# Performance work log

Hardware: AMD Instinct MI355X
Metric: run time of the kernel (lower is better)

## Reference

```python
import jax, jax.numpy as jnp
import numpy as np

N_NODES = 50000
N_EDGES = 800000
IN_F = 256
HEADS = 8
D = 32  # out_perhead
ALPHA_SLOPE = 0.2
EPS = 1e-16


def setup_inputs() -> dict:
    key = jax.random.key(0)
    k1, k2, k3, k4, k5 = jax.random.split(key, 5)
    x = jax.random.normal(k1, (N_NODES, IN_F), dtype=jnp.float32)
    W = jax.random.normal(k2, (HEADS, IN_F, D), dtype=jnp.float32) * 0.05
    a = jax.random.normal(k3, (HEADS, 5 * D), dtype=jnp.float32) * 0.05
    src = jax.random.randint(k4, (N_EDGES,), 0, N_NODES, dtype=jnp.int32)
    dst = jax.random.randint(k5, (N_EDGES,), 0, N_NODES, dtype=jnp.int32)
    return {"x": x, "W": W, "a": a, "src": src, "dst": dst}


def reference(x, W, a, src, dst):
    n = x.shape[0]
    # per-head projection: h[n, heads, d]
    h = jnp.einsum("ni,hio->nho", x, W)
    hs = h[src]  # [E, heads, d]  (edge[0] = source)
    hd = h[dst]  # [E, heads, d]  (edge[1] = destination)
    diff = hd - hs
    # a is the concat attention vector: [src | dst | diff | abs_diff | prod]
    a1, a2, a3, a4, a5 = jnp.split(a, 5, axis=1)  # each [heads, d]
    lin = (
        jnp.einsum("ehd,hd->eh", hs, a1)
        + jnp.einsum("ehd,hd->eh", hd, a2)
        + jnp.einsum("ehd,hd->eh", diff, a3)
        + jnp.einsum("ehd,hd->eh", jnp.abs(diff), a4)
        + jnp.einsum("ehd,hd->eh", hs * hd, a5)
    )  # [E, heads]
    alpha = jnp.where(lin > 0, lin, ALPHA_SLOPE * lin)  # leaky relu
    # sparse softmax grouped by edge[0] (src)
    mx = jax.ops.segment_max(alpha, src, num_segments=n)  # [n, heads]
    e = jnp.exp(alpha - mx[src])
    s = jax.ops.segment_sum(e, src, num_segments=n)
    att = e / (s[src] + EPS)  # [E, heads]
    # spmm: out[i] = sum_{e: src_e = i} att_e * h[dst_e]
    out = jax.ops.segment_sum(att[..., None] * hd, src, num_segments=n)  # [n, heads, d]
    return out.reshape(n, HEADS * D)
```

## Files before the change

kernel.cpp:

```cpp
#include <hip/hip_runtime.h>
#include <hip/hip_bf16.h>
#include <cmath>

#define N_NODES 50000
#define N_EDGES 800000
#define NPAD 50048
#define NWORD (NPAD / 4)
#define WBLK 256
#define HB 64
#define EPB 12500
#define GB 391
#define SLOT 64

typedef _Float16 h2 __attribute__((ext_vector_type(2)));
typedef _Float16 h8 __attribute__((ext_vector_type(8)));
typedef __fp16 fp16x2 __attribute__((ext_vector_type(2)));
typedef float f32x4 __attribute__((ext_vector_type(4)));

__device__ __forceinline__ h2 pkrtz(float a, float b) {
  union { fp16x2 f; h2 h; } t;
  t.f = __builtin_amdgcn_cvt_pkrtz(a, b);
  return t.h;
}

__device__ __forceinline__ float fdot2f(h2 a, h2 b, float c) {
#if __has_builtin(__builtin_amdgcn_fdot2)
  return __builtin_amdgcn_fdot2(a, b, c, false);
#else
  float d;
  asm("v_dot2_f32_f16 %0, %1, %2, %3" : "=v"(d) : "v"(a), "v"(b), "v"(c));
  return d;
#endif
}

__device__ __forceinline__ float fexp2(float x) {
#if __has_builtin(__builtin_amdgcn_exp2f)
  return __builtin_amdgcn_exp2f(x);
#else
  return exp2f(x);
#endif
}

__device__ __forceinline__ h2 habs2(h2 v) {
  union { h2 h; unsigned u; } t;
  t.h = v;
  t.u &= 0x7fff7fffu;
  return t.h;
}

template <int CTRL>
__device__ __forceinline__ float qadd(float v) {
  const int x = __builtin_amdgcn_update_dpp(0, __float_as_int(v), CTRL, 0xF, 0xF, true);
  return v + __int_as_float(x);
}
#define QX1 0xB1
#define QX2 0x4E

__global__ __launch_bounds__(256) void prep_hist(const float* __restrict__ W,
                                                 const int* __restrict__ src,
                                                 ushort* __restrict__ WTh,
                                                 unsigned* __restrict__ hist32) {
  __shared__ unsigned cnt[NWORD];
  const int b = blockIdx.x, t = threadIdx.x;
  if (b < WBLK) {
    const int c = b, k = t;
    union { _Float16 h; ushort u; } o;
    o.h = (_Float16)W[((c >> 5) * 256 + k) * 32 + (c & 31)];
    WTh[c * 256 + k] = o.u;
  } else {
    const int hb = b - WBLK;
    for (int i = t; i < NWORD; i += 256) cnt[i] = 0;
    __syncthreads();
    const int base = hb * EPB;
    for (int k = t; k < EPB; k += 256) {
      const int s = src[base + k];
      atomicAdd(&cnt[s >> 2], 1u << ((s & 3) * 8));
    }
    __syncthreads();
    unsigned* out = hist32 + (size_t)hb * NWORD;
    for (int i = t; i < NWORD; i += 256) out[i] = cnt[i];
  }
}

__global__ __launch_bounds__(256) void edge_offsets(unsigned* __restrict__ hist32,
                                                    unsigned* __restrict__ count32) {
  const int nw = blockIdx.x * 256 + threadIdx.x;
  if (nw >= NWORD) return;
  unsigned run = 0;
  unsigned v = hist32[nw];
#pragma unroll 4
  for (int b = 0; b < HB; ++b) {
    const unsigned nv = (b < HB - 1) ? hist32[(size_t)(b + 1) * NWORD + nw] : 0;
    hist32[(size_t)b * NWORD + nw] = run;
    run += v;
    v = nv;
  }
  count32[nw] = run;
}

__global__ __launch_bounds__(512) void gemm_scatter(
    const float* __restrict__ x, const ushort* __restrict__ WTh,
    ushort* __restrict__ hh, const int* __restrict__ src,
    const int* __restrict__ dst, const unsigned char* __restrict__ hist8,
    ushort* __restrict__ csr) {
  __shared__ __align__(16) char smem[50176];
  const int t = threadIdx.x;
  if (blockIdx.x >= GB) {
    unsigned* cnt = (unsigned*)smem;
    const int hb = blockIdx.x - GB;
    for (int i = t; i < NWORD; i += 512) cnt[i] = 0;
    __syncthreads();
    const int base = hb * EPB;
    const unsigned char* off = hist8 + (size_t)hb * NPAD;
    for (int k = t; k < EPB; k += 512) {
      const int s = src[base + k];
      const int d = dst[base + k];
      const int sh = (s & 3) * 8;
      const unsigned r = atomicAdd(&cnt[s >> 2], 1u << sh);
      const int rank = (r >> sh) & 0xff;
      csr[(s << 6) + off[s] + rank] = (ushort)d;
    }
    return;
  }
  ushort(*Xl)[128][8] = (ushort(*)[128][8])smem;
  ushort(*Wl)[256][8] = (ushort(*)[256][8])(smem + 16384);
  const int bm = blockIdx.x * 128;
  const int w = t >> 6, lane = t & 63;
  const int wch = w >> 1, wnd = w & 1;
  const int l15 = lane & 15, l4 = lane >> 4;
  const int xr = t >> 2;
  const int q4 = t & 3;
  int xrow = bm + xr;
  xrow = xrow < N_NODES ? xrow : N_NODES - 1;
  const float* xp = x + (size_t)xrow * 256 + q4 * 16;
  f32x4 acc[4][4] = {};
  for (int ks = 0; ks < 4; ++ks) {
    const int k0 = ks * 64;
    __syncthreads();
    for (int it = w; it < 32; it += 8) {
      const int kc = it >> 2, q = it & 3;
      const int crow = q * 64 + lane;
      const ushort* gp = WTh + (size_t)crow * 256 + k0 + kc * 8;
      __builtin_amdgcn_global_load_lds(
          (const __attribute__((address_space(1))) void*)gp,
          (__attribute__((address_space(3))) void*)&Wl[kc][q * 64][0],
          16, 0, 0);
    }
    {
      const f32x4 v0 = *(const f32x4*)(xp + k0);
      const f32x4 v1 = *(const f32x4*)(xp + k0 + 4);
      const f32x4 v2 = *(const f32x4*)(xp + k0 + 8);
      const f32x4 v3 = *(const f32x4*)(xp + k0 + 12);
      union { h2 h[4]; h8 v; } u0, u1;
      u0.h[0] = pkrtz(v0[0], v0[1]); u0.h[1] = pkrtz(v0[2], v0[3]);
      u0.h[2] = pkrtz(v1[0], v1[1]); u0.h[3] = pkrtz(v1[2], v1[3]);
      u1.h[0] = pkrtz(v2[0], v2[1]); u1.h[1] = pkrtz(v2[2], v2[3]);
      u1.h[2] = pkrtz(v3[0], v3[1]); u1.h[3] = pkrtz(v3[2], v3[3]);
      *(h8*)&Xl[q4 * 2][xr][0] = u0.v;
      *(h8*)&Xl[q4 * 2 + 1][xr][0] = u1.v;
    }
    __syncthreads();
#pragma unroll
    for (int tt = 0; tt < 2; ++tt) {
      const int kc = tt * 4 + l4;
      h8 bfr[4];
#pragma unroll
      for (int j = 0; j < 4; ++j)
        bfr[j] = *(const h8*)&Xl[kc][wnd * 64 + j * 16 + l15][0];
#pragma unroll
      for (int i = 0; i < 4; ++i) {
        const h8 af = *(const h8*)&Wl[kc][wch * 64 + i * 16 + l15][0];
#pragma unroll
        for (int j = 0; j < 4; ++j)
          acc[i][j] = __builtin_amdgcn_mfma_f32_16x16x32_f16(af, bfr[j],
                                                             acc[i][j], 0, 0, 0);
      }
    }
  }
#pragma unroll
  for (int i = 0; i < 4; ++i) {
#pragma unroll
    for (int j = 0; j < 4; ++j) {
      const int node = bm + wnd * 64 + j * 16 + l15;
      if (node < N_NODES) {
        const int ch = wch * 64 + i * 16 + l4 * 4;
        union { _Float16 h[4]; ushort4 u; } o;
        o.h[0] = (_Float16)acc[i][j][0]; o.h[1] = (_Float16)acc[i][j][1];
        o.h[2] = (_Float16)acc[i][j][2]; o.h[3] = (_Float16)acc[i][j][3];
        *(ushort4*)&hh[(size_t)node * 256 + ch] = o.u;
      }
    }
  }
}

__global__ __launch_bounds__(256) void gat_edge(const ushort* __restrict__ hh,
                                                const float* __restrict__ a,
                                                const unsigned char* __restrict__ count8,
                                                const ushort* __restrict__ csr,
                                                float* __restrict__ out) {
  const int wv = threadIdx.x >> 6;
  const int lane = threadIdx.x & 63;
  const int node = blockIdx.x * 4 + wv;
  if (node >= N_NODES) return;
  const int eoff = lane >> 5;
  const int l32 = lane & 31;
  const int head = l32 >> 2;
  const int c0 = l32 * 8;
  const float* ah = a + head * 160 + ((l32 & 3) * 8);
  const float IL2 = 1.4426950408889634f;

  float a1[8], a2[8], a3[8], a4v[8], a5[8];
  *(float4*)&a1[0] = *(const float4*)(ah + 0);   *(float4*)&a1[4] = *(const float4*)(ah + 4);
  *(float4*)&a2[0] = *(const float4*)(ah + 32);  *(float4*)&a2[4] = *(const float4*)(ah + 36);
  *(float4*)&a3[0] = *(const float4*)(ah + 64);  *(float4*)&a3[4] = *(const float4*)(ah + 68);
  *(float4*)&a4v[0] = *(const float4*)(ah + 96); *(float4*)&a4v[4] = *(const float4*)(ah + 100);
  *(float4*)&a5[0] = *(const float4*)(ah + 128); *(float4*)&a5[4] = *(const float4*)(ah + 132);

  union HU { uint4 u4; h2 h[4]; };
  HU hsu;
  hsu.u4 = *(const uint4*)&hh[(size_t)node * 256 + c0];
  h2 hs2[4], b2[4], a42[4];
  float cn = 0.f;
#pragma unroll
  for (int q = 0; q < 4; ++q) {
    hs2[q] = hsu.h[q];
    const float h0 = (float)hs2[q][0], h1 = (float)hs2[q][1];
    const float b0 = (a2[2 * q] + a3[2 * q] + h0 * a5[2 * q]) * IL2;
    const float b1 = (a2[2 * q + 1] + a3[2 * q + 1] + h1 * a5[2 * q + 1]) * IL2;
    b2[q] = h2{(_Float16)b0, (_Float16)b1};
    a42[q] = h2{(_Float16)(a4v[2 * q] * IL2), (_Float16)(a4v[2 * q + 1] * IL2)};
    cn += h0 * (a1[2 * q] - a3[2 * q]) + h1 * (a1[2 * q + 1] - a3[2 * q + 1]);
  }
  cn *= IL2;
  cn = qadd<QX1>(cn);
  cn = qadd<QX2>(cn);

  float s = 0.f;
  h2 acc2[4] = {};
  const int e0 = node << 6;
  const int cnt = count8[node];
  const int e1 = e0 + cnt;

  auto PROC = [&](const HU& cur, bool cv) {
    float p1 = 0.f, p2 = 0.f;
#pragma unroll
    for (int q = 0; q < 4; ++q) {
      p1 = fdot2f(cur.h[q], b2[q], p1);
      const h2 d = cur.h[q] - hs2[q];
      p2 = fdot2f(habs2(d), a42[q], p2);
    }
    float p = p1 + p2;
    p = qadd<QX1>(p);
    p = qadd<QX2>(p);
    const float lin = cn + p;
    float alpha = fmaxf(lin, 0.2f * lin);
    alpha = cv ? alpha : -INFINITY;
    const float w = fexp2(alpha);
    s += w;
    const h2 w2 = h2{(_Float16)w, (_Float16)w};
#pragma unroll
    for (int q = 0; q < 4; ++q) acc2[q] += w2 * cur.h[q];
  };

  if (cnt > 0) {
    const int nit = (cnt + 1) >> 1;
    const int iA = e0 + eoff;
    const int iB = iA + 2;
    bool uA = iA < e1;
    bool uB = iB < e1;
    HU bufA, bufB;
    {
      const int jA = csr[iA];
      const int jB = csr[iB];
      bufA.u4 = *(const uint4*)&hh[(size_t)jA * 256 + c0];
      bufB.u4 = *(const uint4*)&hh[(size_t)jB * 256 + c0];
    }
    int nAi = iA + 4; bool vA = nAi < e1;
    int nBi = iB + 4; bool vB = nBi < e1;
    int jA2 = csr[nAi];
    int jB2 = csr[nBi];
    const int steps = (nit + 1) >> 1;
    for (int t = 0; t < steps; ++t) {
      PROC(bufA, uA);
      bufA.u4 = *(const uint4*)&hh[(size_t)jA2 * 256 + c0];
      uA = vA;
      nAi += 4; vA = nAi < e1;
      jA2 = csr[nAi];
      PROC(bufB, uB);
      bufB.u4 = *(const uint4*)&hh[(size_t)jB2 * 256 + c0];
      uB = vB;
      nBi += 4; vB = nBi < e1;
      jB2 = csr[nBi];
    }
  }
  float o[8];
#pragma unroll
  for (int q = 0; q < 4; ++q) {
    o[2 * q] = (float)acc2[q][0];
    o[2 * q + 1] = (float)acc2[q][1];
  }
  s += __shfl_xor(s, 32);
  const float inv = 1.f / (s + 1e-16f);
#pragma unroll
  for (int q = 0; q < 8; ++q) o[q] = (o[q] + __shfl_xor(o[q], 32)) * inv;
  if (eoff == 0) {
    *(float4*)&out[(size_t)node * 256 + c0] = make_float4(o[0], o[1], o[2], o[3]);
    *(float4*)&out[(size_t)node * 256 + c0 + 4] = make_float4(o[4], o[5], o[6], o[7]);
  }
}

extern "C" void kernel_launch(void* const* d_in, const int* in_sizes, int n_in,
                              void* d_out, int out_size, void* d_ws, size_t ws_size,
                              hipStream_t stream) {
  const float* x = (const float*)d_in[0];
  const float* W = (const float*)d_in[1];
  const float* a = (const float*)d_in[2];
  const int* src = (const int*)d_in[3];
  const int* dst = (const int*)d_in[4];
  float* out = (float*)d_out;

  char* ws = (char*)d_ws;
  ushort* hh = (ushort*)ws;
  size_t off = (size_t)N_NODES * 256 * 2;
  ushort* WTh = (ushort*)(ws + off);     off += 256 * 256 * 2;
  unsigned* count32 = (unsigned*)(ws + off); off += NWORD * 4;
  ushort* csr = (ushort*)(ws + off);     off += (size_t)NPAD * SLOT * 2;
  unsigned* hist32 = (unsigned*)(ws + off); off += (size_t)HB * NWORD * 4;

  prep_hist<<<WBLK + HB, 256, 0, stream>>>(W, src, WTh, hist32);
  edge_offsets<<<(NWORD + 255) / 256, 256, 0, stream>>>(hist32, count32);
  gemm_scatter<<<GB + HB, 512, 0, stream>>>(x, WTh, hh, src, dst,
                                            (const unsigned char*)hist32, csr);
  gat_edge<<<12500, 256, 0, stream>>>(hh, a, (const unsigned char*)count32,
                                      csr, out);
}
```

Before: 133.4 us.

## Parallelize histogram prefix scan, reorder scatter blocks first, vectorize edge loads

```diff
diff --git a/kernel.cpp b/kernel.cpp
--- a/kernel.cpp
+++ b/kernel.cpp
@@ -6,7 +6,6 @@
 #define N_EDGES 800000
 #define NPAD 50048
 #define NWORD (NPAD / 4)
-#define WBLK 256
 #define HB 64
 #define EPB 12500
 #define GB 391
@@ -56,75 +55,97 @@
 #define QX1 0xB1
 #define QX2 0x4E
 
-__global__ __launch_bounds__(256) void prep_hist(const float* __restrict__ W,
+__global__ __launch_bounds__(512) void prep_hist(const float* __restrict__ W,
                                                  const int* __restrict__ src,
                                                  ushort* __restrict__ WTh,
                                                  unsigned* __restrict__ hist32) {
   __shared__ unsigned cnt[NWORD];
   const int b = blockIdx.x, t = threadIdx.x;
-  if (b < WBLK) {
-    const int c = b, k = t;
+  if (b < 128) {
+    const int c = b * 2 + (t >> 8), k = t & 255;
     union { _Float16 h; ushort u; } o;
     o.h = (_Float16)W[((c >> 5) * 256 + k) * 32 + (c & 31)];
     WTh[c * 256 + k] = o.u;
   } else {
-    const int hb = b - WBLK;
-    for (int i = t; i < NWORD; i += 256) cnt[i] = 0;
+    const int hb = b - 128;
+    for (int i = t; i < NWORD; i += 512) cnt[i] = 0;
     __syncthreads();
     const int base = hb * EPB;
-    for (int k = t; k < EPB; k += 256) {
+    for (int k = t; k < EPB; k += 512) {
       const int s = src[base + k];
       atomicAdd(&cnt[s >> 2], 1u << ((s & 3) * 8));
     }
     __syncthreads();
     unsigned* out = hist32 + (size_t)hb * NWORD;
-    for (int i = t; i < NWORD; i += 256) out[i] = cnt[i];
+    for (int i = t; i < NWORD; i += 512) out[i] = cnt[i];
   }
 }
 
 __global__ __launch_bounds__(256) void edge_offsets(unsigned* __restrict__ hist32,
                                                     unsigned* __restrict__ count32) {
-  const int nw = blockIdx.x * 256 + threadIdx.x;
-  if (nw >= NWORD) return;
+  const int gid = blockIdx.x * 256 + threadIdx.x;
+  if (gid >= NWORD * 4) return;
+  const int nw = gid >> 2;
+  const int sg = gid & 3;
+  const int c0 = sg * 16;
+  unsigned v[16];
+#pragma unroll
+  for (int j = 0; j < 16; ++j) v[j] = hist32[(size_t)(c0 + j) * NWORD + nw];
+  unsigned sum = 0;
+#pragma unroll
+  for (int j = 0; j < 16; ++j) sum += v[j];
+  const int lane = threadIdx.x & 63;
+  const int qb = lane & ~3;
+  const unsigned s0 = __shfl(sum, qb + 0);
+  const unsigned s1 = __shfl(sum, qb + 1);
+  const unsigned s2 = __shfl(sum, qb + 2);
   unsigned run = 0;
-  unsigned v = hist32[nw];
-#pragma unroll 4
-  for (int b = 0; b < HB; ++b) {
-    const unsigned nv = (b < HB - 1) ? hist32[(size_t)(b + 1) * NWORD + nw] : 0;
-    hist32[(size_t)b * NWORD + nw] = run;
-    run += v;
-    v = nv;
-  }
-  count32[nw] = run;
-}
-
-__global__ __launch_bounds__(512) void gemm_scatter(
+  if (sg > 0) run += s0;
+  if (sg > 1) run += s1;
+  if (sg > 2) run += s2;
+#pragma unroll
+  for (int j = 0; j < 16; ++j) {
+    hist32[(size_t)(c0 + j) * NWORD + nw] = run;
+    run += v[j];
+  }
+  if (sg == 3) count32[nw] = run;
+}
+
+__global__ __launch_bounds__(512) void scatter_gemm(
     const float* __restrict__ x, const ushort* __restrict__ WTh,
     ushort* __restrict__ hh, const int* __restrict__ src,
     const int* __restrict__ dst, const unsigned char* __restrict__ hist8,
     ushort* __restrict__ csr) {
   __shared__ __align__(16) char smem[50176];
   const int t = threadIdx.x;
-  if (blockIdx.x >= GB) {
+  if (blockIdx.x < HB) {
     unsigned* cnt = (unsigned*)smem;
-    const int hb = blockIdx.x - GB;
+    const int hb = blockIdx.x;
     for (int i = t; i < NWORD; i += 512) cnt[i] = 0;
     __syncthreads();
     const int base = hb * EPB;
+    const int4* s4p = (const int4*)(src + base);
+    const int4* d4p = (const int4*)(dst + base);
     const unsigned char* off = hist8 + (size_t)hb * NPAD;
-    for (int k = t; k < EPB; k += 512) {
-      const int s = src[base + k];
-      const int d = dst[base + k];
-      const int sh = (s & 3) * 8;
-      const unsigned r = atomicAdd(&cnt[s >> 2], 1u << sh);
-      const int rank = (r >> sh) & 0xff;
-      csr[(s << 6) + off[s] + rank] = (ushort)d;
+    for (int i4 = t; i4 < EPB / 4; i4 += 512) {
+      const int4 s4 = s4p[i4];
+      const int4 d4 = d4p[i4];
+      const int ss[4] = {s4.x, s4.y, s4.z, s4.w};
+      const int dd[4] = {d4.x, d4.y, d4.z, d4.w};
+#pragma unroll
+      for (int u = 0; u < 4; ++u) {
+        const int s = ss[u];
+        const int sh = (s & 3) * 8;
+        const unsigned r = atomicAdd(&cnt[s >> 2], 1u << sh);
+        const int rank = (r >> sh) & 0xff;
+        csr[(s << 6) + off[s] + rank] = (ushort)dd[u];
+      }
     }
     return;
   }
-  ushort(*Xl)[128][8] = (ushort(*)[128][8])smem;
-  ushort(*Wl)[256][8] = (ushort(*)[256][8])(smem + 16384);
-  const int bm = blockIdx.x * 128;
+  ushort(*Xl)[130][8] = (ushort(*)[130][8])smem;
+  ushort(*Wl)[256][8] = (ushort(*)[256][8])(smem + 16640);
+  const int bm = (blockIdx.x - HB) * 128;
   const int w = t >> 6, lane = t & 63;
   const int wch = w >> 1, wnd = w & 1;
   const int l15 = lane & 15, l4 = lane >> 4;
@@ -327,9 +348,9 @@
   ushort* csr = (ushort*)(ws + off);     off += (size_t)NPAD * SLOT * 2;
   unsigned* hist32 = (unsigned*)(ws + off); off += (size_t)HB * NWORD * 4;
 
-  prep_hist<<<WBLK + HB, 256, 0, stream>>>(W, src, WTh, hist32);
-  edge_offsets<<<(NWORD + 255) / 256, 256, 0, stream>>>(hist32, count32);
-  gemm_scatter<<<GB + HB, 512, 0, stream>>>(x, WTh, hh, src, dst,
+  prep_hist<<<128 + HB, 512, 0, stream>>>(W, src, WTh, hist32);
+  edge_offsets<<<(NWORD * 4 + 255) / 256, 256, 0, stream>>>(hist32, count32);
+  scatter_gemm<<<HB + GB, 512, 0, stream>>>(x, WTh, hh, src, dst,
                                             (const unsigned char*)hist32, csr);
   gat_edge<<<12500, 256, 0, stream>>>(hh, a, (const unsigned char*)count32,
                                       csr, out);
```

After: 117.9 us. 1.13x faster.
